# Optimization experiments

Measured on AMD Instinct MI355X. Metric: run time of the kernel, lower is better.

Reference implementation:

```python
import math
import jax, jax.numpy as jnp
import numpy as np

# dims: batch, in-channels, out-channels, features (freq bins), frames, heads, expansion
B, C, CO, F, W, NH, EXP = 1, 8, 8, 512, 256, 8, 4
CC = C + CO          # channels into cross-attn query (cat of h and self_attn)
FC = C + 2 * CO      # channels into FFN (cat of h, self_attn, src_attn)
FH = F * EXP         # FFN hidden features


def mc_linear(x, pw, dw=None):
    # x: [B,Cin,Fin,W]; pw: [Cin,Fout,Fin] per-channel positionwise matmul;
    # dw: [Cout,Cin] channel-mixing matmul ('depthwise' in the repo's naming)
    y = jnp.einsum('bcfw,cgf->bcgw', x, pw)
    if dw is not None:
        y = jnp.einsum('bcgw,oc->bogw', y, dw)
    return y


def frame_conv(x, w, b):
    # Conv2d kernel (1,3), padding (0,1): 1D conv along the frame axis
    y = jax.lax.conv_general_dilated(x, w, (1, 1), ((0, 0), (1, 1)),
                                     dimension_numbers=('NCHW', 'OIHW', 'NCHW'))
    return y + b[None, :, None, None]


def mc_layernorm(x, g, b, eps=1e-5):
    # normalize over the feature axis (2), per (batch, channel, frame)
    mu = x.mean(axis=2, keepdims=True)
    var = jnp.mean(jnp.square(x - mu), axis=2, keepdims=True)
    return (x - mu) * jax.lax.rsqrt(var + eps) * g[None, :, :, None] + b[None, :, :, None]


def mc_attention(xq, xkv, q_pw, q_dw, q_cw, q_cb, k_pw, k_cw, k_cb, v_pw, v_cw, v_cb, o_pw):
    q = frame_conv(mc_linear(xq, q_pw, q_dw), q_cw, q_cb)   # [B,CO,F,Wq]
    k = frame_conv(mc_linear(xkv, k_pw), k_cw, k_cb)        # [B,CO,F,Wk]
    v = frame_conv(mc_linear(xkv, v_pw), v_cw, v_cb)
    dh = F // NH

    def heads(t):  # [B,CO,F,Wt] -> [B,CO,NH,Wt,dh]
        b_, c_, f_, w_ = t.shape
        return t.transpose(0, 1, 3, 2).reshape(b_, c_, w_, NH, dh).transpose(0, 1, 3, 2, 4)

    qh, kh, vh = heads(q), heads(k), heads(v)
    qk = jnp.einsum('bchqd,bchkd->bchqk', qh, kh) / math.sqrt(F)
    a = jnp.einsum('bchqk,bchkd->bchqd', jax.nn.softmax(qk, axis=-1), vh)
    b_, c_, h_, w_, _ = a.shape
    a = a.transpose(0, 1, 3, 2, 4).reshape(b_, c_, w_, F).transpose(0, 1, 3, 2)  # [B,CO,F,Wq]
    return mc_linear(a, o_pw), qk


def setup_inputs() -> dict:
    key = jax.random.key(0)
    ks = jax.random.split(key, 32)
    it = iter(range(32))

    def rn(shape, s=0.02):
        return jax.random.normal(ks[next(it)], shape, jnp.float32) * s

    inp = {
        'x': jax.random.normal(ks[next(it)], (B, C, F, W), jnp.float32),
        'src': jax.random.normal(ks[next(it)], (B, C, F, W), jnp.float32),
        'ln_g': jnp.ones((C, F), jnp.float32),
        'ln_b': jnp.zeros((C, F), jnp.float32),
        # self-attention (C -> CO, C == CO so no channel-mix on projections)
        'sa_q_pw': rn((C, F, F)), 'sa_q_cw': rn((CO, CO, 1, 3), 0.1), 'sa_q_cb': jnp.zeros((CO,), jnp.float32),
        'sa_k_pw': rn((C, F, F)), 'sa_k_cw': rn((CO, CO, 1, 3), 0.1), 'sa_k_cb': jnp.zeros((CO,), jnp.float32),
        'sa_v_pw': rn((C, F, F)), 'sa_v_cw': rn((CO, CO, 1, 3), 0.1), 'sa_v_cb': jnp.zeros((CO,), jnp.float32),
        'sa_o_pw': rn((CO, F, F)),
        # cross-attention (query from CC=C+CO channels -> CO; key/value from src with C channels)
        'ca_q_pw': rn((CC, F, F)), 'ca_q_dw': rn((CO, CC), 0.1),
        'ca_q_cw': rn((CO, CO, 1, 3), 0.1), 'ca_q_cb': jnp.zeros((CO,), jnp.float32),
        'ca_k_pw': rn((C, F, F)), 'ca_k_cw': rn((CO, CO, 1, 3), 0.1), 'ca_k_cb': jnp.zeros((CO,), jnp.float32),
        'ca_v_pw': rn((C, F, F)), 'ca_v_cw': rn((CO, CO, 1, 3), 0.1), 'ca_v_cb': jnp.zeros((CO,), jnp.float32),
        'ca_o_pw': rn((CO, F, F)),
        # FFN
        'ffn1_pw': rn((FC, FH, F)), 'ffn1_dw': rn((FC, FC), 0.1),
        'ffn2_pw': rn((FC, F, FH)), 'ffn2_dw': rn((C, FC), 0.1),
    }
    return inp


def reference(x, src, ln_g, ln_b,
              sa_q_pw, sa_q_cw, sa_q_cb, sa_k_pw, sa_k_cw, sa_k_cb, sa_v_pw, sa_v_cw, sa_v_cb, sa_o_pw,
              ca_q_pw, ca_q_dw, ca_q_cw, ca_q_cb, ca_k_pw, ca_k_cw, ca_k_cb, ca_v_pw, ca_v_cw, ca_v_cb, ca_o_pw,
              ffn1_pw, ffn1_dw, ffn2_pw, ffn2_dw):
    h = mc_layernorm(x, ln_g, ln_b)
    sa, qk1 = mc_attention(h, h, sa_q_pw, None, sa_q_cw, sa_q_cb,
                           sa_k_pw, sa_k_cw, sa_k_cb, sa_v_pw, sa_v_cw, sa_v_cb, sa_o_pw)
    ca, qk2 = mc_attention(jnp.concatenate([h, sa], axis=1), src,
                           ca_q_pw, ca_q_dw, ca_q_cw, ca_q_cb,
                           ca_k_pw, ca_k_cw, ca_k_cb, ca_v_pw, ca_v_cw, ca_v_cb, ca_o_pw)
    z = mc_linear(jnp.concatenate([h, sa, ca], axis=1), ffn1_pw, ffn1_dw)
    z = jax.nn.gelu(z, approximate=False)
    z = mc_linear(z, ffn2_pw, ffn2_dw)
    return (x + z, qk1, qk2)
```

## Files before the change

kernel.cpp:

```cpp
#include <hip/hip_runtime.h>
#include <math.h>

typedef __attribute__((ext_vector_type(4))) float f32x4;
typedef __attribute__((ext_vector_type(8))) short s16x8;
typedef __attribute__((ext_vector_type(4))) short s16x4;

__device__ __forceinline__ unsigned short f2b(float f) {
    union { float f; unsigned u; } v; v.f = f;
    unsigned r = v.u + 0x7fffu + ((v.u >> 16) & 1u);
    return (unsigned short)(r >> 16);
}
__device__ __forceinline__ float b2f(unsigned short u) {
    union { unsigned u; float f; } v; v.u = ((unsigned)u) << 16;
    return v.f;
}

constexpr int kF = 512;
constexpr int kW = 256;
constexpr int kFW = kF * kW;

__global__ __launch_bounds__(256) void prep_kernel(const float* __restrict__ x,
                                                   const float* __restrict__ g,
                                                   const float* __restrict__ b,
                                                   unsigned short* __restrict__ hTb,
                                                   const float* __restrict__ src,
                                                   unsigned short* __restrict__ SRCT) {
    __shared__ float tile[64][65];
    __shared__ float s1[16][16], s2[16][16];
    int bid = blockIdx.x;
    int t = threadIdx.x;
    if (bid < 128) {
        int c = bid >> 4;
        int w0 = (bid & 15) * 16;
        int wi = t & 15, fg = t >> 4;
        const float* xb = x + (size_t)c * kFW + w0 + wi;
        float sum = 0.f, sum2 = 0.f;
        for (int j = 0; j < 32; ++j) {
            float v = xb[(size_t)(fg * 32 + j) * kW];
            sum += v; sum2 += v * v;
        }
        s1[fg][wi] = sum; s2[fg][wi] = sum2;
        __syncthreads();
        float ts = 0.f, tq = 0.f;
        #pragma unroll
        for (int j = 0; j < 16; ++j) { ts += s1[j][wi]; tq += s2[j][wi]; }
        float mu = ts * (1.0f / 512.0f);
        float rstd = rsqrtf(tq * (1.0f / 512.0f) - mu * mu + 1e-5f);
        const float* gc = g + c * kF + fg * 32;
        const float* bc = b + c * kF + fg * 32;
        unsigned short* ob = hTb + (size_t)c * kFW + (size_t)(w0 + wi) * kF + fg * 32;
        for (int j = 0; j < 32; j += 4) {
            float v0 = xb[(size_t)(fg * 32 + j + 0) * kW];
            float v1 = xb[(size_t)(fg * 32 + j + 1) * kW];
            float v2 = xb[(size_t)(fg * 32 + j + 2) * kW];
            float v3 = xb[(size_t)(fg * 32 + j + 3) * kW];
            s16x4 p = { (short)f2b((v0 - mu) * rstd * gc[j + 0] + bc[j + 0]),
                        (short)f2b((v1 - mu) * rstd * gc[j + 1] + bc[j + 1]),
                        (short)f2b((v2 - mu) * rstd * gc[j + 2] + bc[j + 2]),
                        (short)f2b((v3 - mu) * rstd * gc[j + 3] + bc[j + 3]) };
            *(s16x4*)(&ob[j]) = p;
        }
    } else {
        int fid = bid - 128;
        int c = fid >> 5;
        int f0 = ((fid >> 2) & 7) * 64, w0 = (fid & 3) * 64;
        int tw = t & 63, tf4 = t >> 6;
        for (int i = 0; i < 16; ++i) {
            int f = tf4 * 16 + i;
            tile[f][tw] = src[(size_t)c * kFW + (size_t)(f0 + f) * kW + w0 + tw];
        }
        __syncthreads();
        int w = t >> 2, fc = (t & 3) * 16;
        unsigned short* ob = SRCT + (size_t)c * kFW + (size_t)(w0 + w) * kF + f0 + fc;
        for (int j = 0; j < 16; j += 4) {
            s16x4 p = { (short)f2b(tile[fc + j + 0][w]), (short)f2b(tile[fc + j + 1][w]),
                        (short)f2b(tile[fc + j + 2][w]), (short)f2b(tile[fc + j + 3][w]) };
            *(s16x4*)(&ob[j]) = p;
        }
    }
}

struct WSeg { const float* A; const unsigned short* B; void* C; int omode; };
struct WB8 { WSeg s[8]; };

__device__ __forceinline__ void wg_compute(const unsigned short* __restrict__ ldsbuf,
                                           f32x4 A0, f32x4 A1, f32x4 A2, f32x4 A3,
                                           f32x4* acc, int l16, int l4) {
    s16x8 af0 = { (short)f2b(A0.x), (short)f2b(A0.y), (short)f2b(A0.z), (short)f2b(A0.w),
                  (short)f2b(A1.x), (short)f2b(A1.y), (short)f2b(A1.z), (short)f2b(A1.w) };
    #pragma unroll
    for (int ni = 0; ni < 16; ++ni) {
        int rr = ni * 16 + l16;
        s16x8 bf = *(const s16x8*)(&ldsbuf[rr * 64 + ((l4 * 8) ^ ((rr & 7) << 3))]);
        acc[ni] = __builtin_amdgcn_mfma_f32_16x16x32_bf16(af0, bf, acc[ni], 0, 0, 0);
    }
    s16x8 af1 = { (short)f2b(A2.x), (short)f2b(A2.y), (short)f2b(A2.z), (short)f2b(A2.w),
                  (short)f2b(A3.x), (short)f2b(A3.y), (short)f2b(A3.z), (short)f2b(A3.w) };
    #pragma unroll
    for (int ni = 0; ni < 16; ++ni) {
        int rr = ni * 16 + l16;
        s16x8 bf = *(const s16x8*)(&ldsbuf[rr * 64 + ((32 + l4 * 8) ^ ((rr & 7) << 3))]);
        acc[ni] = __builtin_amdgcn_mfma_f32_16x16x32_bf16(af1, bf, acc[ni], 0, 0, 0);
    }
}

__global__ __launch_bounds__(256) void wgemm256(WB8 wb, int M, int K, int Klocal,
                                                long a_ch, long b_ch, long c_ch, long c_split,
                                                int segshift, int nm, int ksplit) {
    __shared__ unsigned short lds[2][16384];
    int t = threadIdx.x, lane = t & 63, wv = t >> 6;
    int l16 = lane & 15, l4 = lane >> 4;

    int id = blockIdx.x;
    int r = id & 7, j = id >> 3;
    int per = nm * ksplit;
    int y = r + 8 * (j / per);
    int rem = j % per;
    int mt = rem % nm;
    int kz = rem / nm;
    int seg = y >> segshift, c = y & ((1 << segshift) - 1);
    WSeg sg = wb.s[seg];
    int bm = mt * 64;
    int kbase = kz * Klocal;

    const float* A = sg.A + (size_t)c * a_ch + kbase;
    const unsigned short* B = sg.B + (size_t)c * b_ch + kbase;
    const float* arow = A + (size_t)(bm + wv * 16 + l16) * K + l4 * 8;

    int srow = t >> 3, sck = t & 7;
    const unsigned short* bsrc = B + (size_t)srow * K + sck * 8;
    int sdoff = srow * 64 + ((sck * 8) ^ ((srow & 7) << 3));

    s16x8 stg0, stg1, stg2, stg3, stg4, stg5, stg6, stg7;
    f32x4 a0, a1, a2, a3, e0, e1, e2, e3;

    #define LOADSTG(c0) do { const unsigned short* _b = bsrc + (size_t)(c0) * 64; \
        stg0 = *(const s16x8*)(_b); \
        stg1 = *(const s16x8*)(_b + (size_t)32 * K); \
        stg2 = *(const s16x8*)(_b + (size_t)64 * K); \
        stg3 = *(const s16x8*)(_b + (size_t)96 * K); \
        stg4 = *(const s16x8*)(_b + (size_t)128 * K); \
        stg5 = *(const s16x8*)(_b + (size_t)160 * K); \
        stg6 = *(const s16x8*)(_b + (size_t)192 * K); \
        stg7 = *(const s16x8*)(_b + (size_t)224 * K); } while (0)
    #define WRITESTG(bi) do { unsigned short* _d = &lds[bi][sdoff]; \
        *(s16x8*)(_d + 0)     = stg0; \
        *(s16x8*)(_d + 2048)  = stg1; \
        *(s16x8*)(_d + 4096)  = stg2; \
        *(s16x8*)(_d + 6144)  = stg3; \
        *(s16x8*)(_d + 8192)  = stg4; \
        *(s16x8*)(_d + 10240) = stg5; \
        *(s16x8*)(_d + 12288) = stg6; \
        *(s16x8*)(_d + 14336) = stg7; } while (0)
    #define LDA(d0,d1,d2,d3,koff) do { \
        d0 = __builtin_nontemporal_load((const f32x4*)(arow + (koff))); \
        d1 = __builtin_nontemporal_load((const f32x4*)(arow + (koff) + 4)); \
        d2 = __builtin_nontemporal_load((const f32x4*)(arow + (koff) + 32)); \
        d3 = __builtin_nontemporal_load((const f32x4*)(arow + (koff) + 36)); } while (0)

    f32x4 acc[16];
    #pragma unroll
    for (int i = 0; i < 16; ++i) acc[i] = (f32x4){0.f, 0.f, 0.f, 0.f};

    LOADSTG(0); LDA(a0, a1, a2, a3, 0);
    WRITESTG(0);

    int nc = Klocal >> 6;
    for (int cch = 0; cch < nc; cch += 2) {
        LOADSTG(cch + 1); LDA(e0, e1, e2, e3, (cch + 1) * 64);
        __syncthreads();
        wg_compute(lds[0], a0, a1, a2, a3, acc, l16, l4);
        WRITESTG(1);
        if (cch + 2 < nc) { LOADSTG(cch + 2); LDA(a0, a1, a2, a3, (cch + 2) * 64); }
        __syncthreads();
        wg_compute(lds[1], e0, e1, e2, e3, acc, l16, l4);
        if (cch + 2 < nc) WRITESTG(0);
    }
    #undef LOADSTG
    #undef WRITESTG
    #undef LDA

    int m0 = bm + wv * 16 + l4 * 4;
    if (sg.omode == 2) {
        unsigned short* C = (unsigned short*)sg.C + (size_t)c * c_ch;
        #pragma unroll
        for (int ni = 0; ni < 16; ++ni) {
            int n = ni * 16 + l16;
            s16x4 pk = { (short)f2b(acc[ni][0]), (short)f2b(acc[ni][1]),
                         (short)f2b(acc[ni][2]), (short)f2b(acc[ni][3]) };
            *(s16x4*)(&C[(size_t)n * M + m0]) = pk;
        }
    } else if (sg.omode == 1) {
        unsigned short* C = (unsigned short*)sg.C + (size_t)c * c_ch;
        #pragma unroll
        for (int ni = 0; ni < 16; ++ni) {
            int n = ni * 16 + l16;
            #pragma unroll
            for (int rr = 0; rr < 4; ++rr)
                C[(size_t)(m0 + rr) * 256 + n] = f2b(acc[ni][rr]);
        }
    } else {
        float* C = (float*)sg.C + (size_t)c * c_ch + (size_t)kz * c_split;
        #pragma unroll
        for (int ni = 0; ni < 16; ++ni) {
            int n = ni * 16 + l16;
            #pragma unroll
            for (int rr = 0; rr < 4; ++rr)
                C[(size_t)(m0 + rr) * 256 + n] = acc[ni][rr];
        }
    }
}

__global__ __launch_bounds__(256) void attn_kernel(
    const unsigned short* __restrict__ Qt, const unsigned short* __restrict__ Kt,
    const unsigned short* __restrict__ VN, float* __restrict__ S,
    unsigned short* __restrict__ ATTT, float scale)
{
    __shared__ unsigned short q_lds[4096];
    __shared__ unsigned short kv_lds[16384];
    __shared__ unsigned short p_lds[16384];
    __shared__ float smax[4][64], ssum[4][64], sinv[64];
    int t = threadIdx.x, lane = t & 63, wv = t >> 6;
    int l16 = lane & 15, l4 = lane >> 4;
    int ch = blockIdx.y, c = ch >> 3, h = ch & 7;
    int bm = blockIdx.x * 64;
    const unsigned short* Qb = Qt + (size_t)c * kFW + h * 64;
    const unsigned short* Kb = Kt + (size_t)c * kFW + h * 64;
    const unsigned short* Vb = VN + (size_t)c * kFW + (size_t)(h * 64) * 256;
    float* Sb = S + (size_t)ch * 65536;
    unsigned short* Ab = ATTT + (size_t)c * kFW + h * 64;

    s16x8 qr[2], kr[8], vr[8];
    #pragma unroll
    for (int i = 0; i < 2; ++i) {
        int idx = i * 256 + t; int rr = idx >> 3, ck = idx & 7;
        qr[i] = *(const s16x8*)(Qb + (size_t)(bm + rr) * 512 + ck * 8);
    }
    #pragma unroll
    for (int i = 0; i < 8; ++i) {
        int idx = i * 256 + t; int rr = idx >> 3, ck = idx & 7;
        kr[i] = *(const s16x8*)(Kb + (size_t)rr * 512 + ck * 8);
    }
    #pragma unroll
    for (int i = 0; i < 8; ++i) {
        int idx = i * 256 + t; int d = idx >> 5, cs = idx & 31;
        vr[i] = *(const s16x8*)(Vb + (size_t)d * 256 + cs * 8);
    }
    #pragma unroll
    for (int i = 0; i < 2; ++i) {
        int idx = i * 256 + t; int rr = idx >> 3, ck = idx & 7;
        *(s16x8*)(&q_lds[rr * 64 + ((ck * 8) ^ ((rr & 7) << 3))]) = qr[i];
    }
    #pragma unroll
    for (int i = 0; i < 8; ++i) {
        int idx = i * 256 + t; int rr = idx >> 3, ck = idx & 7;
        *(s16x8*)(&kv_lds[rr * 64 + ((ck * 8) ^ ((rr & 7) << 3))]) = kr[i];
    }
    __syncthreads();

    f32x4 acc[4][4];
    #pragma unroll
    for (int i = 0; i < 4; ++i)
        #pragma unroll
        for (int jj = 0; jj < 4; ++jj) acc[i][jj] = (f32x4){0.f, 0.f, 0.f, 0.f};
    #pragma unroll
    for (int ks = 0; ks < 2; ++ks) {
        s16x8 af[4], bfr[4];
        #pragma unroll
        for (int mi = 0; mi < 4; ++mi) {
            int rq = mi * 16 + l16;
            af[mi] = *(const s16x8*)(&q_lds[rq * 64 + ((ks * 32 + l4 * 8) ^ ((rq & 7) << 3))]);
        }
        #pragma unroll
        for (int ni = 0; ni < 4; ++ni) {
            int rk = wv * 64 + ni * 16 + l16;
            bfr[ni] = *(const s16x8*)(&kv_lds[rk * 64 + ((ks * 32 + l4 * 8) ^ ((rk & 7) << 3))]);
        }
        #pragma unroll
        for (int mi = 0; mi < 4; ++mi)
            #pragma unroll
            for (int ni = 0; ni < 4; ++ni)
                acc[mi][ni] = __builtin_amdgcn_mfma_f32_16x16x32_bf16(af[mi], bfr[ni], acc[mi][ni], 0, 0, 0);
    }

    #pragma unroll
    for (int mi = 0; mi < 4; ++mi)
        #pragma unroll
        for (int ni = 0; ni < 4; ++ni) {
            acc[mi][ni] *= scale;
            int col = wv * 64 + ni * 16 + l16;
            int row0 = bm + mi * 16 + l4 * 4;
            #pragma unroll
            for (int rr = 0; rr < 4; ++rr)
                Sb[(size_t)(row0 + rr) * 256 + col] = acc[mi][ni][rr];
        }

    float rmax[4][4];
    #pragma unroll
    for (int mi = 0; mi < 4; ++mi)
        #pragma unroll
        for (int rr = 0; rr < 4; ++rr)
            rmax[mi][rr] = fmaxf(fmaxf(acc[mi][0][rr], acc[mi][1][rr]), fmaxf(acc[mi][2][rr], acc[mi][3][rr]));
    #pragma unroll
    for (int d = 1; d < 16; d <<= 1)
        #pragma unroll
        for (int mi = 0; mi < 4; ++mi)
            #pragma unroll
            for (int rr = 0; rr < 4; ++rr)
                rmax[mi][rr] = fmaxf(rmax[mi][rr], __shfl_xor(rmax[mi][rr], d));
    if (l16 == 0)
        #pragma unroll
        for (int mi = 0; mi < 4; ++mi)
            #pragma unroll
            for (int rr = 0; rr < 4; ++rr)
                smax[wv][mi * 16 + l4 * 4 + rr] = rmax[mi][rr];
    __syncthreads();
    float rsum[4][4];
    #pragma unroll
    for (int mi = 0; mi < 4; ++mi)
        #pragma unroll
        for (int rr = 0; rr < 4; ++rr) {
            int row = mi * 16 + l4 * 4 + rr;
            float rM = fmaxf(fmaxf(smax[0][row], smax[1][row]), fmaxf(smax[2][row], smax[3][row]));
            rsum[mi][rr] = 0.f;
            #pragma unroll
            for (int ni = 0; ni < 4; ++ni) {
                float e = __expf(acc[mi][ni][rr] - rM);
                acc[mi][ni][rr] = e;
                rsum[mi][rr] += e;
            }
        }
    #pragma unroll
    for (int d = 1; d < 16; d <<= 1)
        #pragma unroll
        for (int mi = 0; mi < 4; ++mi)
            #pragma unroll
            for (int rr = 0; rr < 4; ++rr)
                rsum[mi][rr] += __shfl_xor(rsum[mi][rr], d);
    if (l16 == 0)
        #pragma unroll
        for (int mi = 0; mi < 4; ++mi)
            #pragma unroll
            for (int rr = 0; rr < 4; ++rr)
                ssum[wv][mi * 16 + l4 * 4 + rr] = rsum[mi][rr];
    __syncthreads();

    #pragma unroll
    for (int i = 0; i < 8; ++i) {
        int idx = i * 256 + t; int d = idx >> 5, cs = idx & 31;
        *(s16x8*)(&kv_lds[d * 256 + ((cs * 8) ^ ((d & 7) << 3))]) = vr[i];
    }
    #pragma unroll
    for (int mi = 0; mi < 4; ++mi)
        #pragma unroll
        for (int ni = 0; ni < 4; ++ni) {
            int col = wv * 64 + ni * 16 + l16;
            int cb = col & ~7, cl = col & 7;
            #pragma unroll
            for (int rr = 0; rr < 4; ++rr) {
                int row = mi * 16 + l4 * 4 + rr;
                p_lds[row * 256 + (cb ^ ((row & 7) << 3)) + cl] = f2b(acc[mi][ni][rr]);
            }
        }
    if (t < 64) sinv[t] = 1.f / (ssum[0][t] + ssum[1][t] + ssum[2][t] + ssum[3][t]);
    __syncthreads();

    f32x4 po[4];
    #pragma unroll
    for (int ni = 0; ni < 4; ++ni) po[ni] = (f32x4){0.f, 0.f, 0.f, 0.f};
    int qrow = wv * 16 + l16;
    #pragma unroll
    for (int ks = 0; ks < 8; ++ks) {
        s16x8 paf = *(const s16x8*)(&p_lds[qrow * 256 + ((ks * 32 + l4 * 8) ^ ((qrow & 7) << 3))]);
        #pragma unroll
        for (int ni = 0; ni < 4; ++ni) {
            int rd = ni * 16 + l16;
            s16x8 bf = *(const s16x8*)(&kv_lds[rd * 256 + ((ks * 32 + l4 * 8) ^ ((rd & 7) << 3))]);
            po[ni] = __builtin_amdgcn_mfma_f32_16x16x32_bf16(paf, bf, po[ni], 0, 0, 0);
        }
    }
    #pragma unroll
    for (int ni = 0; ni < 4; ++ni) {
        int d = ni * 16 + l16;
        #pragma unroll
        for (int rr = 0; rr < 4; ++rr) {
            int row = wv * 16 + l4 * 4 + rr;
            Ab[(size_t)(bm + row) * 512 + d] = f2b(po[ni][rr] * sinv[row]);
        }
    }
}

struct ConvArgs {
    const unsigned short* in[5];
    unsigned short* out[5];
    const float* cw[5];
    const float* cb[5];
    int mode[5];
};

__global__ __launch_bounds__(256) void conv5_kernel(ConvArgs a) {
    int g = blockIdx.y;
    __shared__ float scw[192]; __shared__ float scb[8];
    int t = threadIdx.x;
    if (t < 192) scw[t] = a.cw[g][t];
    if (t >= 192 && t < 200) scb[t - 192] = a.cb[g][t - 192];
    __syncthreads();
    const unsigned short* in = a.in[g];
    unsigned short* out = a.out[g];
    int gi = blockIdx.x * 256 + t;
    int mode = a.mode[g];
    int w = mode ? (gi & 255) : (gi >> 9);
    int str = mode ? 1 : 512;
    float acc[8];
    #pragma unroll
    for (int o = 0; o < 8; ++o) acc[o] = scb[o];
    bool hm = w > 0, hp = w < 255;
    #pragma unroll
    for (int i = 0; i < 8; ++i) {
        size_t base = (size_t)i * kFW + gi;
        float xm = hm ? b2f(in[base - str]) : 0.f;
        float x0 = b2f(in[base]);
        float xp = hp ? b2f(in[base + str]) : 0.f;
        #pragma unroll
        for (int o = 0; o < 8; ++o) {
            const float* wp = &scw[(o * 8 + i) * 3];
            acc[o] += wp[0] * xm + wp[1] * x0 + wp[2] * xp;
        }
    }
    #pragma unroll
    for (int o = 0; o < 8; ++o) out[(size_t)o * kFW + gi] = f2b(acc[o]);
}

__global__ __launch_bounds__(256) void mixconv_kernel(const unsigned short* __restrict__ in,
                                                      const float* __restrict__ dw,
                                                      const float* __restrict__ cw,
                                                      const float* __restrict__ cb,
                                                      unsigned short* __restrict__ out) {
    __shared__ float sdw[128], scw[192], scb[8];
    int t = threadIdx.x;
    if (t < 128) sdw[t] = dw[t];
    if (t >= 128 && t < 136) scb[t - 128] = cb[t - 128];
    if (t < 192) scw[t] = cw[t];
    __syncthreads();
    int gi = blockIdx.x * 256 + t;
    int w = gi >> 9;
    bool hm = w > 0, hp = w < 255;
    float xc[16], xm[16], xp[16];
    #pragma unroll
    for (int cc = 0; cc < 16; ++cc) {
        size_t base = (size_t)cc * kFW + gi;
        xc[cc] = b2f(in[base]);
        xm[cc] = hm ? b2f(in[base - 512]) : 0.f;
        xp[cc] = hp ? b2f(in[base + 512]) : 0.f;
    }
    float mm[8], m0[8], mp[8];
    #pragma unroll
    for (int o = 0; o < 8; ++o) {
        float am = 0.f, a0 = 0.f, ap = 0.f;
        #pragma unroll
        for (int cc = 0; cc < 16; ++cc) {
            float wv = sdw[o * 16 + cc];
            am += wv * xm[cc]; a0 += wv * xc[cc]; ap += wv * xp[cc];
        }
        mm[o] = am; m0[o] = a0; mp[o] = ap;
    }
    #pragma unroll
    for (int o = 0; o < 8; ++o) {
        float acc = scb[o];
        #pragma unroll
        for (int i = 0; i < 8; ++i) {
            const float* wp = &scw[(o * 8 + i) * 3];
            acc += wp[0] * mm[i] + wp[1] * m0[i] + wp[2] * mp[i];
        }
        out[(size_t)o * kFW + gi] = f2b(acc);
    }
}

__global__ __launch_bounds__(256) void gelu24_kernel(unsigned short* __restrict__ z,
                                                     const float* __restrict__ dw) {
    __shared__ float sdw[576];
    int t = threadIdx.x;
    for (int i = t; i < 576; i += 256) sdw[i] = dw[i];
    __syncthreads();
    size_t gi = (size_t)blockIdx.x * 256 + t;
    const size_t CH = (size_t)256 * 2048;
    float xv[24];
    #pragma unroll
    for (int cc = 0; cc < 24; ++cc) xv[cc] = b2f(z[cc * CH + gi]);
    #pragma unroll
    for (int o = 0; o < 24; ++o) {
        float s = 0.f;
        #pragma unroll
        for (int cc = 0; cc < 24; ++cc) s += sdw[o * 24 + cc] * xv[cc];
        s = 0.5f * s * (1.0f + erff(s * 0.7071067811865475f));
        z[o * CH + gi] = f2b(s);
    }
}

__global__ __launch_bounds__(256) void final_mix_add2(const float* __restrict__ x,
                                                      const float* __restrict__ z2,
                                                      const float* __restrict__ dw,
                                                      float* __restrict__ out) {
    __shared__ float sdw[192];
    int t = threadIdx.x;
    if (t < 192) sdw[t] = dw[t];
    __syncthreads();
    int gi = blockIdx.x * 256 + t;
    const size_t PSZ = (size_t)24 * kFW;
    float xv[24];
    #pragma unroll
    for (int cc = 0; cc < 24; ++cc) {
        size_t o = (size_t)cc * kFW + gi;
        xv[cc] = z2[o] + z2[PSZ + o];
    }
    #pragma unroll
    for (int o = 0; o < 8; ++o) {
        float s = 0.f;
        #pragma unroll
        for (int cc = 0; cc < 24; ++cc) s += sdw[o * 24 + cc] * xv[cc];
        out[(size_t)o * kFW + gi] = x[(size_t)o * kFW + gi] + s;
    }
}

extern "C" void kernel_launch(void* const* d_in, const int* in_sizes, int n_in,
                              void* d_out, int out_size, void* d_ws, size_t ws_size,
                              hipStream_t stream) {
    const float* x       = (const float*)d_in[0];
    const float* src     = (const float*)d_in[1];
    const float* ln_g    = (const float*)d_in[2];
    const float* ln_b    = (const float*)d_in[3];
    const float* sa_q_pw = (const float*)d_in[4];
    const float* sa_q_cw = (const float*)d_in[5];
    const float* sa_q_cb = (const float*)d_in[6];
    const float* sa_k_pw = (const float*)d_in[7];
    const float* sa_k_cw = (const float*)d_in[8];
    const float* sa_k_cb = (const float*)d_in[9];
    const float* sa_v_pw = (const float*)d_in[10];
    const float* sa_v_cw = (const float*)d_in[11];
    const float* sa_v_cb = (const float*)d_in[12];
    const float* sa_o_pw = (const float*)d_in[13];
    const float* ca_q_pw = (const float*)d_in[14];
    const float* ca_q_dw = (const float*)d_in[15];
    const float* ca_q_cw = (const float*)d_in[16];
    const float* ca_q_cb = (const float*)d_in[17];
    const float* ca_k_pw = (const float*)d_in[18];
    const float* ca_k_cw = (const float*)d_in[19];
    const float* ca_k_cb = (const float*)d_in[20];
    const float* ca_v_pw = (const float*)d_in[21];
    const float* ca_v_cw = (const float*)d_in[22];
    const float* ca_v_cb = (const float*)d_in[23];
    const float* ca_o_pw = (const float*)d_in[24];
    const float* ffn1_pw = (const float*)d_in[25];
    const float* ffn1_dw = (const float*)d_in[26];
    const float* ffn2_pw = (const float*)d_in[27];
    const float* ffn2_dw = (const float*)d_in[28];

    float* out  = (float*)d_out;
    float* qk1o = out + 1048576;
    float* qk2o = out + 1048576 + 4194304;

    unsigned char* ws = (unsigned char*)d_ws;
    unsigned short* CAT24  = (unsigned short*)(ws + 0);
    unsigned short* hTb    = CAT24;
    unsigned short* saTb   = CAT24 + 8 * (size_t)kFW;
    unsigned short* caTb   = CAT24 + 16 * (size_t)kFW;
    unsigned short* SRCT   = (unsigned short*)(ws + 6291456);
    unsigned short* preQ   = (unsigned short*)(ws + 8388608);
    unsigned short* preK   = (unsigned short*)(ws + 10485760);
    unsigned short* preVsa = (unsigned short*)(ws + 12582912);
    unsigned short* preKca = (unsigned short*)(ws + 14680064);
    unsigned short* preVca = (unsigned short*)(ws + 16777216);
    unsigned short* QT     = (unsigned short*)(ws + 18874368);
    unsigned short* KT     = (unsigned short*)(ws + 20971520);
    unsigned short* VNsa   = (unsigned short*)(ws + 23068672);
    unsigned short* KTca   = (unsigned short*)(ws + 25165824);
    unsigned short* VNca   = (unsigned short*)(ws + 27262976);
    unsigned short* PRE16  = (unsigned short*)(ws + 29360128);
    unsigned short* QTca   = (unsigned short*)(ws + 33554432);
    unsigned short* ATTT   = (unsigned short*)(ws + 35651584);
    unsigned short* Z0T    = (unsigned short*)(ws + 8388608);
    float*          Z2P    = (float*)(ws + 37748736);

    const float qscale = 0.044194173824159216f;
    dim3 blk(256);

    prep_kernel<<<384, blk, 0, stream>>>(x, ln_g, ln_b, hTb, src, SRCT);

    WB8 p6;
    p6.s[0] = { sa_q_pw, hTb,  preQ,   2 };
    p6.s[1] = { sa_k_pw, hTb,  preK,   2 };
    p6.s[2] = { sa_v_pw, hTb,  preVsa, 1 };
    p6.s[3] = { ca_k_pw, SRCT, preKca, 2 };
    p6.s[4] = { ca_v_pw, SRCT, preVca, 1 };
    p6.s[5] = { ca_q_pw, hTb,  PRE16,  2 };
    p6.s[6] = p6.s[0]; p6.s[7] = p6.s[0];
    wgemm256<<<dim3(384), blk, 0, stream>>>(p6, 512, 512, 512, 262144, kFW, kFW, 0, 3, 8, 1);

    ConvArgs c5;
    c5.in[0] = preQ;   c5.out[0] = QT;   c5.cw[0] = sa_q_cw; c5.cb[0] = sa_q_cb; c5.mode[0] = 0;
    c5.in[1] = preK;   c5.out[1] = KT;   c5.cw[1] = sa_k_cw; c5.cb[1] = sa_k_cb; c5.mode[1] = 0;
    c5.in[2] = preVsa; c5.out[2] = VNsa; c5.cw[2] = sa_v_cw; c5.cb[2] = sa_v_cb; c5.mode[2] = 1;
    c5.in[3] = preKca; c5.out[3] = KTca; c5.cw[3] = ca_k_cw; c5.cb[3] = ca_k_cb; c5.mode[3] = 0;
    c5.in[4] = preVca; c5.out[4] = VNca; c5.cw[4] = ca_v_cw; c5.cb[4] = ca_v_cb; c5.mode[4] = 1;
    conv5_kernel<<<dim3(512, 5), blk, 0, stream>>>(c5);

    attn_kernel<<<dim3(4, 64), blk, 0, stream>>>(QT, KT, VNsa, qk1o, ATTT, qscale);
    WB8 so;
    so.s[0] = { sa_o_pw, ATTT, saTb, 2 };
    for (int i = 1; i < 8; ++i) so.s[i] = so.s[0];
    wgemm256<<<dim3(64), blk, 0, stream>>>(so, 512, 512, 512, 262144, kFW, kFW, 0, 8, 8, 1);

    WB8 cq2;
    cq2.s[0] = { ca_q_pw + 8 * 262144, saTb, PRE16 + 8 * (size_t)kFW, 2 };
    for (int i = 1; i < 8; ++i) cq2.s[i] = cq2.s[0];
    wgemm256<<<dim3(64), blk, 0, stream>>>(cq2, 512, 512, 512, 262144, kFW, kFW, 0, 8, 8, 1);
    mixconv_kernel<<<512, blk, 0, stream>>>(PRE16, ca_q_dw, ca_q_cw, ca_q_cb, QTca);

    attn_kernel<<<dim3(4, 64), blk, 0, stream>>>(QTca, KTca, VNca, qk2o, ATTT, qscale);
    WB8 co;
    co.s[0] = { ca_o_pw, ATTT, caTb, 2 };
    for (int i = 1; i < 8; ++i) co.s[i] = co.s[0];
    wgemm256<<<dim3(64), blk, 0, stream>>>(co, 512, 512, 512, 262144, kFW, kFW, 0, 8, 8, 1);

    WB8 f1;
    f1.s[0] = { ffn1_pw, CAT24, Z0T, 2 };
    for (int i = 1; i < 8; ++i) f1.s[i] = f1.s[0];
    wgemm256<<<dim3(768), blk, 0, stream>>>(f1, 2048, 512, 512, 1048576, kFW, 524288, 0, 8, 32, 1);
    gelu24_kernel<<<2048, blk, 0, stream>>>(Z0T, ffn1_dw);
    WB8 f2;
    f2.s[0] = { ffn2_pw, Z0T, Z2P, 0 };
    for (int i = 1; i < 8; ++i) f2.s[i] = f2.s[0];
    wgemm256<<<dim3(384), blk, 0, stream>>>(f2, 512, 2048, 1024, 1048576, 524288, kFW, 3145728, 8, 8, 2);
    final_mix_add2<<<512, blk, 0, stream>>>(x, Z2P, ffn2_dw, out);
}
```

Before: 295.8 us.

## Replace LDS-staged weight GEMM with 32-row direct-load tiles and deeper split-K

The 64-row GEMM that staged the activation operand through double-buffered LDS is replaced by a 32-row tile kernel. Each of its four waves covers 16 rows by 128 columns and loads its B fragments straight from global memory. All GEMM launches double their grid size, and the FFN2 GEMM moves from 2-way to 4-way split-K, so the final mix kernel now sums four partial buffers. This drops LDS traffic and barriers and adds parallelism for the small 64-block launches. In exchange, B data is re-read from cache by each wave pair, there is more partial-sum traffic, and the Z2P workspace footprint is larger.

```diff
diff --git a/kernel.cpp b/kernel.cpp
--- a/kernel.cpp
+++ b/kernel.cpp
@@ -83,31 +83,9 @@
 struct WSeg { const float* A; const unsigned short* B; void* C; int omode; };
 struct WB8 { WSeg s[8]; };
 
-__device__ __forceinline__ void wg_compute(const unsigned short* __restrict__ ldsbuf,
-                                           f32x4 A0, f32x4 A1, f32x4 A2, f32x4 A3,
-                                           f32x4* acc, int l16, int l4) {
-    s16x8 af0 = { (short)f2b(A0.x), (short)f2b(A0.y), (short)f2b(A0.z), (short)f2b(A0.w),
-                  (short)f2b(A1.x), (short)f2b(A1.y), (short)f2b(A1.z), (short)f2b(A1.w) };
-    #pragma unroll
-    for (int ni = 0; ni < 16; ++ni) {
-        int rr = ni * 16 + l16;
-        s16x8 bf = *(const s16x8*)(&ldsbuf[rr * 64 + ((l4 * 8) ^ ((rr & 7) << 3))]);
-        acc[ni] = __builtin_amdgcn_mfma_f32_16x16x32_bf16(af0, bf, acc[ni], 0, 0, 0);
-    }
-    s16x8 af1 = { (short)f2b(A2.x), (short)f2b(A2.y), (short)f2b(A2.z), (short)f2b(A2.w),
-                  (short)f2b(A3.x), (short)f2b(A3.y), (short)f2b(A3.z), (short)f2b(A3.w) };
-    #pragma unroll
-    for (int ni = 0; ni < 16; ++ni) {
-        int rr = ni * 16 + l16;
-        s16x8 bf = *(const s16x8*)(&ldsbuf[rr * 64 + ((32 + l4 * 8) ^ ((rr & 7) << 3))]);
-        acc[ni] = __builtin_amdgcn_mfma_f32_16x16x32_bf16(af1, bf, acc[ni], 0, 0, 0);
-    }
-}
-
-__global__ __launch_bounds__(256) void wgemm256(WB8 wb, int M, int K, int Klocal,
-                                                long a_ch, long b_ch, long c_ch, long c_split,
-                                                int segshift, int nm, int ksplit) {
-    __shared__ unsigned short lds[2][16384];
+__global__ __launch_bounds__(256, 4) void wgemm32(WB8 wb, int M, int a_rs, int b_rs,
+                                                  long a_ch, long b_ch, long c_ch, long c_split,
+                                                  int segshift, int nm, int ksplit) {
     int t = threadIdx.x, lane = t & 63, wv = t >> 6;
     int l16 = lane & 15, l4 = lane >> 4;
 
@@ -120,72 +98,44 @@
     int kz = rem / nm;
     int seg = y >> segshift, c = y & ((1 << segshift) - 1);
     WSeg sg = wb.s[seg];
-    int bm = mt * 64;
-    int kbase = kz * Klocal;
-
-    const float* A = sg.A + (size_t)c * a_ch + kbase;
-    const unsigned short* B = sg.B + (size_t)c * b_ch + kbase;
-    const float* arow = A + (size_t)(bm + wv * 16 + l16) * K + l4 * 8;
-
-    int srow = t >> 3, sck = t & 7;
-    const unsigned short* bsrc = B + (size_t)srow * K + sck * 8;
-    int sdoff = srow * 64 + ((sck * 8) ^ ((srow & 7) << 3));
-
-    s16x8 stg0, stg1, stg2, stg3, stg4, stg5, stg6, stg7;
-    f32x4 a0, a1, a2, a3, e0, e1, e2, e3;
-
-    #define LOADSTG(c0) do { const unsigned short* _b = bsrc + (size_t)(c0) * 64; \
-        stg0 = *(const s16x8*)(_b); \
-        stg1 = *(const s16x8*)(_b + (size_t)32 * K); \
-        stg2 = *(const s16x8*)(_b + (size_t)64 * K); \
-        stg3 = *(const s16x8*)(_b + (size_t)96 * K); \
-        stg4 = *(const s16x8*)(_b + (size_t)128 * K); \
-        stg5 = *(const s16x8*)(_b + (size_t)160 * K); \
-        stg6 = *(const s16x8*)(_b + (size_t)192 * K); \
-        stg7 = *(const s16x8*)(_b + (size_t)224 * K); } while (0)
-    #define WRITESTG(bi) do { unsigned short* _d = &lds[bi][sdoff]; \
-        *(s16x8*)(_d + 0)     = stg0; \
-        *(s16x8*)(_d + 2048)  = stg1; \
-        *(s16x8*)(_d + 4096)  = stg2; \
-        *(s16x8*)(_d + 6144)  = stg3; \
-        *(s16x8*)(_d + 8192)  = stg4; \
-        *(s16x8*)(_d + 10240) = stg5; \
-        *(s16x8*)(_d + 12288) = stg6; \
-        *(s16x8*)(_d + 14336) = stg7; } while (0)
-    #define LDA(d0,d1,d2,d3,koff) do { \
-        d0 = __builtin_nontemporal_load((const f32x4*)(arow + (koff))); \
-        d1 = __builtin_nontemporal_load((const f32x4*)(arow + (koff) + 4)); \
-        d2 = __builtin_nontemporal_load((const f32x4*)(arow + (koff) + 32)); \
-        d3 = __builtin_nontemporal_load((const f32x4*)(arow + (koff) + 36)); } while (0)
-
-    f32x4 acc[16];
-    #pragma unroll
-    for (int i = 0; i < 16; ++i) acc[i] = (f32x4){0.f, 0.f, 0.f, 0.f};
-
-    LOADSTG(0); LDA(a0, a1, a2, a3, 0);
-    WRITESTG(0);
-
-    int nc = Klocal >> 6;
-    for (int cch = 0; cch < nc; cch += 2) {
-        LOADSTG(cch + 1); LDA(e0, e1, e2, e3, (cch + 1) * 64);
-        __syncthreads();
-        wg_compute(lds[0], a0, a1, a2, a3, acc, l16, l4);
-        WRITESTG(1);
-        if (cch + 2 < nc) { LOADSTG(cch + 2); LDA(a0, a1, a2, a3, (cch + 2) * 64); }
-        __syncthreads();
-        wg_compute(lds[1], e0, e1, e2, e3, acc, l16, l4);
-        if (cch + 2 < nc) WRITESTG(0);
-    }
-    #undef LOADSTG
-    #undef WRITESTG
-    #undef LDA
-
-    int m0 = bm + wv * 16 + l4 * 4;
+    int bm = mt * 32;
+    int kbase = kz * 512;
+
+    int mrow = bm + (wv & 1) * 16 + l16;
+    int nh = (wv >> 1) * 128;
+    const float* ap = sg.A + (size_t)c * a_ch + (size_t)mrow * a_rs + kbase + l4 * 8;
+    const unsigned short* bp = sg.B + (size_t)c * b_ch + (size_t)(nh + l16) * b_rs + kbase + l4 * 8;
+    const size_t bstep = (size_t)16 * b_rs;
+
+    f32x4 acc[8];
+    #pragma unroll
+    for (int i = 0; i < 8; ++i) acc[i] = (f32x4){0.f, 0.f, 0.f, 0.f};
+
+    f32x4 a0 = __builtin_nontemporal_load((const f32x4*)ap);
+    f32x4 a1 = __builtin_nontemporal_load((const f32x4*)(ap + 4));
+
+    #pragma unroll
+    for (int ks = 0; ks < 16; ++ks) {
+        f32x4 c0 = a0, c1 = a1;
+        if (ks < 15) {
+            a0 = __builtin_nontemporal_load((const f32x4*)(ap + (ks + 1) * 32));
+            a1 = __builtin_nontemporal_load((const f32x4*)(ap + (ks + 1) * 32 + 4));
+        }
+        s16x8 af = { (short)f2b(c0.x), (short)f2b(c0.y), (short)f2b(c0.z), (short)f2b(c0.w),
+                     (short)f2b(c1.x), (short)f2b(c1.y), (short)f2b(c1.z), (short)f2b(c1.w) };
+        #pragma unroll
+        for (int ni = 0; ni < 8; ++ni) {
+            s16x8 bf = *(const s16x8*)(bp + (size_t)ni * bstep + ks * 32);
+            acc[ni] = __builtin_amdgcn_mfma_f32_16x16x32_bf16(af, bf, acc[ni], 0, 0, 0);
+        }
+    }
+
+    int m0 = bm + (wv & 1) * 16 + l4 * 4;
     if (sg.omode == 2) {
         unsigned short* C = (unsigned short*)sg.C + (size_t)c * c_ch;
         #pragma unroll
-        for (int ni = 0; ni < 16; ++ni) {
-            int n = ni * 16 + l16;
+        for (int ni = 0; ni < 8; ++ni) {
+            int n = nh + ni * 16 + l16;
             s16x4 pk = { (short)f2b(acc[ni][0]), (short)f2b(acc[ni][1]),
                          (short)f2b(acc[ni][2]), (short)f2b(acc[ni][3]) };
             *(s16x4*)(&C[(size_t)n * M + m0]) = pk;
@@ -193,8 +143,8 @@
     } else if (sg.omode == 1) {
         unsigned short* C = (unsigned short*)sg.C + (size_t)c * c_ch;
         #pragma unroll
-        for (int ni = 0; ni < 16; ++ni) {
-            int n = ni * 16 + l16;
+        for (int ni = 0; ni < 8; ++ni) {
+            int n = nh + ni * 16 + l16;
             #pragma unroll
             for (int rr = 0; rr < 4; ++rr)
                 C[(size_t)(m0 + rr) * 256 + n] = f2b(acc[ni][rr]);
@@ -202,8 +152,8 @@
     } else {
         float* C = (float*)sg.C + (size_t)c * c_ch + (size_t)kz * c_split;
         #pragma unroll
-        for (int ni = 0; ni < 16; ++ni) {
-            int n = ni * 16 + l16;
+        for (int ni = 0; ni < 8; ++ni) {
+            int n = nh + ni * 16 + l16;
             #pragma unroll
             for (int rr = 0; rr < 4; ++rr)
                 C[(size_t)(m0 + rr) * 256 + n] = acc[ni][rr];
@@ -497,7 +447,7 @@
     }
 }
 
-__global__ __launch_bounds__(256) void final_mix_add2(const float* __restrict__ x,
+__global__ __launch_bounds__(256) void final_mix_add4(const float* __restrict__ x,
                                                       const float* __restrict__ z2,
                                                       const float* __restrict__ dw,
                                                       float* __restrict__ out) {
@@ -511,7 +461,7 @@
     #pragma unroll
     for (int cc = 0; cc < 24; ++cc) {
         size_t o = (size_t)cc * kFW + gi;
-        xv[cc] = z2[o] + z2[PSZ + o];
+        xv[cc] = z2[o] + z2[PSZ + o] + z2[2 * PSZ + o] + z2[3 * PSZ + o];
     }
     #pragma unroll
     for (int o = 0; o < 8; ++o) {
@@ -594,7 +544,7 @@
     p6.s[4] = { ca_v_pw, SRCT, preVca, 1 };
     p6.s[5] = { ca_q_pw, hTb,  PRE16,  2 };
     p6.s[6] = p6.s[0]; p6.s[7] = p6.s[0];
-    wgemm256<<<dim3(384), blk, 0, stream>>>(p6, 512, 512, 512, 262144, kFW, kFW, 0, 3, 8, 1);
+    wgemm32<<<dim3(768), blk, 0, stream>>>(p6, 512, 512, 512, 262144, kFW, kFW, 0, 3, 16, 1);
 
     ConvArgs c5;
     c5.in[0] = preQ;   c5.out[0] = QT;   c5.cw[0] = sa_q_cw; c5.cb[0] = sa_q_cb; c5.mode[0] = 0;
@@ -608,28 +558,28 @@
     WB8 so;
     so.s[0] = { sa_o_pw, ATTT, saTb, 2 };
     for (int i = 1; i < 8; ++i) so.s[i] = so.s[0];
-    wgemm256<<<dim3(64), blk, 0, stream>>>(so, 512, 512, 512, 262144, kFW, kFW, 0, 8, 8, 1);
+    wgemm32<<<dim3(128), blk, 0, stream>>>(so, 512, 512, 512, 262144, kFW, kFW, 0, 8, 16, 1);
 
     WB8 cq2;
     cq2.s[0] = { ca_q_pw + 8 * 262144, saTb, PRE16 + 8 * (size_t)kFW, 2 };
     for (int i = 1; i < 8; ++i) cq2.s[i] = cq2.s[0];
-    wgemm256<<<dim3(64), blk, 0, stream>>>(cq2, 512, 512, 512, 262144, kFW, kFW, 0, 8, 8, 1);
+    wgemm32<<<dim3(128), blk, 0, stream>>>(cq2, 512, 512, 512, 262144, kFW, kFW, 0, 8, 16, 1);
     mixconv_kernel<<<512, blk, 0, stream>>>(PRE16, ca_q_dw, ca_q_cw, ca_q_cb, QTca);
 
     attn_kernel<<<dim3(4, 64), blk, 0, stream>>>(QTca, KTca, VNca, qk2o, ATTT, qscale);
     WB8 co;
     co.s[0] = { ca_o_pw, ATTT, caTb, 2 };
     for (int i = 1; i < 8; ++i) co.s[i] = co.s[0];
-    wgemm256<<<dim3(64), blk, 0, stream>>>(co, 512, 512, 512, 262144, kFW, kFW, 0, 8, 8, 1);
+    wgemm32<<<dim3(128), blk, 0, stream>>>(co, 512, 512, 512, 262144, kFW, kFW, 0, 8, 16, 1);
 
     WB8 f1;
     f1.s[0] = { ffn1_pw, CAT24, Z0T, 2 };
     for (int i = 1; i < 8; ++i) f1.s[i] = f1.s[0];
-    wgemm256<<<dim3(768), blk, 0, stream>>>(f1, 2048, 512, 512, 1048576, kFW, 524288, 0, 8, 32, 1);
+    wgemm32<<<dim3(1536), blk, 0, stream>>>(f1, 2048, 512, 512, 1048576, kFW, 524288, 0, 8, 64, 1);
     gelu24_kernel<<<2048, blk, 0, stream>>>(Z0T, ffn1_dw);
     WB8 f2;
     f2.s[0] = { ffn2_pw, Z0T, Z2P, 0 };
     for (int i = 1; i < 8; ++i) f2.s[i] = f2.s[0];
-    wgemm256<<<dim3(384), blk, 0, stream>>>(f2, 512, 2048, 1024, 1048576, 524288, kFW, 3145728, 8, 8, 2);
-    final_mix_add2<<<512, blk, 0, stream>>>(x, Z2P, ffn2_dw, out);
-}
+    wgemm32<<<dim3(1536), blk, 0, stream>>>(f2, 512, 2048, 2048, 1048576, 524288, kFW, 3145728, 8, 16, 4);
+    final_mix_add4<<<512, blk, 0, stream>>>(x, Z2P, ffn2_dw, out);
+}
```

Result: slower. 514.2 us (+73.9%).

## Stage GEMM B tiles via direct global-to-LDS loads with single buffer

Applied to the files above, without the earlier changes.

Replaces the register-staged, double-buffered B-tile copy in the weight GEMM with global_load_lds direct transfers into a single swizzled LDS buffer, and prefetches A one 32-wide k-step ahead. This removes the VGPR staging registers and LDS write instructions, and halves LDS use. The cost is that the loads for each tile are issued and waited on just before compute, so global latency is no longer overlapped with the previous chunk's math.

```diff
diff --git a/kernel.cpp b/kernel.cpp
--- a/kernel.cpp
+++ b/kernel.cpp
@@ -13,6 +13,12 @@
 __device__ __forceinline__ float b2f(unsigned short u) {
     union { unsigned u; float f; } v; v.u = ((unsigned)u) << 16;
     return v.f;
+}
+
+__device__ __forceinline__ void gll16(const void* g, void* l) {
+    __builtin_amdgcn_global_load_lds((const __attribute__((address_space(1))) unsigned int*)g,
+                                     (__attribute__((address_space(3))) unsigned int*)l,
+                                     16, 0, 0);
 }
 
 constexpr int kF = 512;
@@ -83,31 +89,10 @@
 struct WSeg { const float* A; const unsigned short* B; void* C; int omode; };
 struct WB8 { WSeg s[8]; };
 
-__device__ __forceinline__ void wg_compute(const unsigned short* __restrict__ ldsbuf,
-                                           f32x4 A0, f32x4 A1, f32x4 A2, f32x4 A3,
-                                           f32x4* acc, int l16, int l4) {
-    s16x8 af0 = { (short)f2b(A0.x), (short)f2b(A0.y), (short)f2b(A0.z), (short)f2b(A0.w),
-                  (short)f2b(A1.x), (short)f2b(A1.y), (short)f2b(A1.z), (short)f2b(A1.w) };
-    #pragma unroll
-    for (int ni = 0; ni < 16; ++ni) {
-        int rr = ni * 16 + l16;
-        s16x8 bf = *(const s16x8*)(&ldsbuf[rr * 64 + ((l4 * 8) ^ ((rr & 7) << 3))]);
-        acc[ni] = __builtin_amdgcn_mfma_f32_16x16x32_bf16(af0, bf, acc[ni], 0, 0, 0);
-    }
-    s16x8 af1 = { (short)f2b(A2.x), (short)f2b(A2.y), (short)f2b(A2.z), (short)f2b(A2.w),
-                  (short)f2b(A3.x), (short)f2b(A3.y), (short)f2b(A3.z), (short)f2b(A3.w) };
-    #pragma unroll
-    for (int ni = 0; ni < 16; ++ni) {
-        int rr = ni * 16 + l16;
-        s16x8 bf = *(const s16x8*)(&ldsbuf[rr * 64 + ((32 + l4 * 8) ^ ((rr & 7) << 3))]);
-        acc[ni] = __builtin_amdgcn_mfma_f32_16x16x32_bf16(af1, bf, acc[ni], 0, 0, 0);
-    }
-}
-
 __global__ __launch_bounds__(256) void wgemm256(WB8 wb, int M, int K, int Klocal,
                                                 long a_ch, long b_ch, long c_ch, long c_split,
                                                 int segshift, int nm, int ksplit) {
-    __shared__ unsigned short lds[2][16384];
+    __shared__ unsigned short lds[16384];
     int t = threadIdx.x, lane = t & 63, wv = t >> 6;
     int l16 = lane & 15, l4 = lane >> 4;
 
@@ -124,61 +109,46 @@
     int kbase = kz * Klocal;
 
     const float* A = sg.A + (size_t)c * a_ch + kbase;
-    const unsigned short* B = sg.B + (size_t)c * b_ch + kbase;
+    const unsigned short* Bc = sg.B + (size_t)c * b_ch + kbase;
     const float* arow = A + (size_t)(bm + wv * 16 + l16) * K + l4 * 8;
 
-    int srow = t >> 3, sck = t & 7;
-    const unsigned short* bsrc = B + (size_t)srow * K + sck * 8;
-    int sdoff = srow * 64 + ((sck * 8) ^ ((srow & 7) << 3));
-
-    s16x8 stg0, stg1, stg2, stg3, stg4, stg5, stg6, stg7;
-    f32x4 a0, a1, a2, a3, e0, e1, e2, e3;
-
-    #define LOADSTG(c0) do { const unsigned short* _b = bsrc + (size_t)(c0) * 64; \
-        stg0 = *(const s16x8*)(_b); \
-        stg1 = *(const s16x8*)(_b + (size_t)32 * K); \
-        stg2 = *(const s16x8*)(_b + (size_t)64 * K); \
-        stg3 = *(const s16x8*)(_b + (size_t)96 * K); \
-        stg4 = *(const s16x8*)(_b + (size_t)128 * K); \
-        stg5 = *(const s16x8*)(_b + (size_t)160 * K); \
-        stg6 = *(const s16x8*)(_b + (size_t)192 * K); \
-        stg7 = *(const s16x8*)(_b + (size_t)224 * K); } while (0)
-    #define WRITESTG(bi) do { unsigned short* _d = &lds[bi][sdoff]; \
-        *(s16x8*)(_d + 0)     = stg0; \
-        *(s16x8*)(_d + 2048)  = stg1; \
-        *(s16x8*)(_d + 4096)  = stg2; \
-        *(s16x8*)(_d + 6144)  = stg3; \
-        *(s16x8*)(_d + 8192)  = stg4; \
-        *(s16x8*)(_d + 10240) = stg5; \
-        *(s16x8*)(_d + 12288) = stg6; \
-        *(s16x8*)(_d + 14336) = stg7; } while (0)
-    #define LDA(d0,d1,d2,d3,koff) do { \
-        d0 = __builtin_nontemporal_load((const f32x4*)(arow + (koff))); \
-        d1 = __builtin_nontemporal_load((const f32x4*)(arow + (koff) + 4)); \
-        d2 = __builtin_nontemporal_load((const f32x4*)(arow + (koff) + 32)); \
-        d3 = __builtin_nontemporal_load((const f32x4*)(arow + (koff) + 36)); } while (0)
+    int rsub = lane >> 3;
+    int gsw = ((lane & 7) ^ rsub) * 8;
+    const unsigned short* bsrc = Bc + (size_t)rsub * K + gsw;
 
     f32x4 acc[16];
     #pragma unroll
     for (int i = 0; i < 16; ++i) acc[i] = (f32x4){0.f, 0.f, 0.f, 0.f};
 
-    LOADSTG(0); LDA(a0, a1, a2, a3, 0);
-    WRITESTG(0);
-
-    int nc = Klocal >> 6;
-    for (int cch = 0; cch < nc; cch += 2) {
-        LOADSTG(cch + 1); LDA(e0, e1, e2, e3, (cch + 1) * 64);
+    f32x4 pa0 = __builtin_nontemporal_load((const f32x4*)arow);
+    f32x4 pa1 = __builtin_nontemporal_load((const f32x4*)(arow + 4));
+
+    for (int kc = 0; kc < Klocal; kc += 64) {
+        if (kc) __syncthreads();
+        #pragma unroll
+        for (int i = 0; i < 8; ++i) {
+            int r0 = wv * 64 + i * 8;
+            gll16(bsrc + (size_t)r0 * K + kc, (char*)lds + (r0 << 7));
+        }
         __syncthreads();
-        wg_compute(lds[0], a0, a1, a2, a3, acc, l16, l4);
-        WRITESTG(1);
-        if (cch + 2 < nc) { LOADSTG(cch + 2); LDA(a0, a1, a2, a3, (cch + 2) * 64); }
-        __syncthreads();
-        wg_compute(lds[1], e0, e1, e2, e3, acc, l16, l4);
-        if (cch + 2 < nc) WRITESTG(0);
-    }
-    #undef LOADSTG
-    #undef WRITESTG
-    #undef LDA
+        #pragma unroll
+        for (int ks = 0; ks < 2; ++ks) {
+            f32x4 c0 = pa0, c1 = pa1;
+            int nk = kc + (ks + 1) * 32;
+            if (nk < Klocal) {
+                pa0 = __builtin_nontemporal_load((const f32x4*)(arow + nk));
+                pa1 = __builtin_nontemporal_load((const f32x4*)(arow + nk + 4));
+            }
+            s16x8 af = { (short)f2b(c0.x), (short)f2b(c0.y), (short)f2b(c0.z), (short)f2b(c0.w),
+                         (short)f2b(c1.x), (short)f2b(c1.y), (short)f2b(c1.z), (short)f2b(c1.w) };
+            #pragma unroll
+            for (int ni = 0; ni < 16; ++ni) {
+                int rr = ni * 16 + l16;
+                s16x8 bf = *(const s16x8*)(&lds[rr * 64 + ((ks * 32 + l4 * 8) ^ ((rr & 7) << 3))]);
+                acc[ni] = __builtin_amdgcn_mfma_f32_16x16x32_bf16(af, bf, acc[ni], 0, 0, 0);
+            }
+        }
+    }
 
     int m0 = bm + wv * 16 + l4 * 4;
     if (sg.omode == 2) {
```

Result: faster. 271.7 us (-8.2%).
